# Performance work log

Measured on AMD Instinct MI355X. Metric: run time of the kernel, lower is better.

The kernel has to match this reference:

```python
import math
import jax, jax.numpy as jnp
import numpy as np

N = 50000   # nodes
E = 200000  # edges
B = 1024    # graphs
D = 256     # d_model
DA = 128    # d_atom_embed
DB = 64     # d_bond_embed
NA = 16     # num_atom_types
NB = 5      # num_bond_types
L = 6       # num_layers
DC = 2      # d_cond
IN0 = DA + 8 + D  # 392, layer-0 input dim


def setup_inputs() -> dict:
    key = jax.random.key(0)
    ks = jax.random.split(key, 48)
    def w(i, shape):
        fan_in = shape[-2] if len(shape) >= 2 else shape[-1]
        return jax.random.normal(ks[i], shape, jnp.float32) / jnp.sqrt(jnp.float32(fan_in))
    inp = {
        'x_noisy': jax.random.randint(ks[0], (N,), 0, NA),
        'node_mask_obs': jax.random.randint(ks[1], (N,), 0, 2),
        'edge_attr_noisy': jax.random.randint(ks[2], (E,), 0, NB),
        'edge_mask_obs': jax.random.randint(ks[3], (E,), 0, 2),
        'edge_index': jax.random.randint(ks[4], (2, E), 0, N),
        't_node': jax.random.randint(ks[5], (N,), 0, 200),
        'cond_vec': jax.random.normal(ks[6], (B, DC), jnp.float32),
        'batch': jnp.sort(jax.random.randint(ks[7], (N,), 0, B)),
        # embeddings
        'atom_emb': w(8, (NA, DA)), 'bond_emb': w(9, (NB, DB)),
        'nmask_emb': w(10, (2, 8)), 'emask_emb': w(11, (2, 8)),
        # timestep MLP
        't_W1': w(12, (D, D)), 't_b1': jnp.zeros((D,)),
        't_W2': w(13, (D, D)), 't_b2': jnp.zeros((D,)),
        # cond projection
        'cond_W': w(14, (DC, D)), 'cond_b': jnp.zeros((D,)),
        # edge MLP
        'edge_W1': w(15, (DB + 8, D)), 'edge_b1': jnp.zeros((D,)),
        'edge_W2': w(16, (D, D)), 'edge_b2': jnp.zeros((D,)),
        # layer-0 edge projection (GINEConv edge_dim -> in_dim)
        'e0_W': w(17, (D, IN0)),
        # layer-0 GINEConv MLP
        'conv0_W1': w(18, (IN0, D)), 'conv0_b1': jnp.zeros((D,)),
        'conv0_W2': w(19, (D, D)), 'conv0_b2': jnp.zeros((D,)),
        'conv0_eps': jnp.zeros(()),
        # layers 1..5 GINEConv MLPs (stacked)
        'convs_W1': w(20, (L - 1, D, D)), 'convs_b1': jnp.zeros((L - 1, D)),
        'convs_W2': w(21, (L - 1, D, D)), 'convs_b2': jnp.zeros((L - 1, D)),
        'convs_eps': jnp.zeros((L - 1,)),
        # BatchNorm (eval mode: running_mean=0, running_var=1)
        'bn_gamma': jnp.ones((L, D)) + 0.1 * jax.random.normal(ks[22], (L, D), jnp.float32),
        'bn_beta': 0.1 * jax.random.normal(ks[23], (L, D), jnp.float32),
        # heads
        'atom_W': w(24, (D, NA)), 'atom_b': jnp.zeros((NA,)),
        'bond_W': w(25, (D, NB)), 'bond_b': jnp.zeros((NB,)),
    }
    return inp


def _sinusoidal(t, d_model):
    half = d_model // 2
    freqs = jnp.exp(jnp.arange(half, dtype=jnp.float32) * (-math.log(10000.0) / max(1, half - 1)))
    angles = t.astype(jnp.float32)[:, None] * freqs[None, :]
    return jnp.concatenate([jnp.sin(angles), jnp.cos(angles)], axis=1)


def _bn_eval(h, gamma, beta, eps=1e-5):
    # running_mean=0, running_var=1
    return h * (gamma / jnp.sqrt(1.0 + eps)) + beta


def reference(x_noisy, node_mask_obs, edge_attr_noisy, edge_mask_obs, edge_index,
              t_node, cond_vec, batch,
              atom_emb, bond_emb, nmask_emb, emask_emb,
              t_W1, t_b1, t_W2, t_b2, cond_W, cond_b,
              edge_W1, edge_b1, edge_W2, edge_b2, e0_W,
              conv0_W1, conv0_b1, conv0_W2, conv0_b2, conv0_eps,
              convs_W1, convs_b1, convs_W2, convs_b2, convs_eps,
              bn_gamma, bn_beta, atom_W, atom_b, bond_W, bond_b):
    silu = jax.nn.silu
    # node features
    x_atom = atom_emb[x_noisy]                       # [N, DA]
    x_mask = nmask_emb[node_mask_obs]                # [N, 8]
    t_emb = _sinusoidal(t_node, D)                   # [N, D]
    t_emb = silu(t_emb @ t_W1 + t_b1) @ t_W2 + t_b2
    c_node = (cond_vec @ cond_W + cond_b)[batch]     # [N, D]
    h = jnp.concatenate([x_atom, x_mask, t_emb + c_node], axis=-1)  # [N, IN0]
    # edge features
    e_in = jnp.concatenate([bond_emb[edge_attr_noisy], emask_emb[edge_mask_obs]], axis=-1)
    e_feat = silu(e_in @ edge_W1 + edge_b1) @ edge_W2 + edge_b2      # [E, D]
    src, dst = edge_index[0], edge_index[1]

    def gine(h, e, eps, W1, b1, W2, b2):
        msg = jax.nn.relu(h[src] + e)                               # [E, d]
        agg = jax.ops.segment_sum(msg, dst, num_segments=N)          # [N, d]
        z = (1.0 + eps) * h + agg
        return silu(z @ W1 + b1) @ W2 + b2

    # layer 0 (edge features projected to IN0)
    h = gine(h, e_feat @ e0_W, conv0_eps, conv0_W1, conv0_b1, conv0_W2, conv0_b2)
    h = silu(_bn_eval(h, bn_gamma[0], bn_beta[0]))  # dropout off (eval)
    # layers 1..5
    for i in range(L - 1):
        h = gine(h, e_feat, convs_eps[i], convs_W1[i], convs_b1[i], convs_W2[i], convs_b2[i])
        h = silu(_bn_eval(h, bn_gamma[i + 1], bn_beta[i + 1]))
    atom_logits = h @ atom_W + atom_b                # [N, NA]
    edge_h = h[src] + h[dst]                          # [E, D]
    bond_logits = edge_h @ bond_W + bond_b            # [E, NB]
    return atom_logits, bond_logits
```

## Files before the change

kernel.cpp:

```cpp
#include <hip/hip_runtime.h>
#include <cstdint>
#include <cmath>

typedef unsigned short u16;
typedef unsigned int   u32;

using bf16x8 = __attribute__((ext_vector_type(8))) short;
using f32x4  = __attribute__((ext_vector_type(4))) float;

#define DM 256
#define W0 448
#define W0_REAL 392

__device__ __forceinline__ float bf2f(u16 v) {
  union { u32 u; float f; } c; c.u = ((u32)v) << 16; return c.f;
}
__device__ __forceinline__ u16 f2bf(float f) {
  union { float f; u32 u; } c; c.f = f;
  u32 u = c.u;
  return (u16)((u + 0x7FFFu + ((u >> 16) & 1u)) >> 16);
}
__device__ __forceinline__ float siluf(float y) {
  return y / (1.0f + __expf(-y));
}
__device__ __forceinline__ uint4 pack8(float f0, float f1, float f2, float f3,
                                       float f4, float f5, float f6, float f7) {
  uint4 o;
  o.x = (u32)f2bf(f0) | ((u32)f2bf(f1) << 16);
  o.y = (u32)f2bf(f2) | ((u32)f2bf(f3) << 16);
  o.z = (u32)f2bf(f4) | ((u32)f2bf(f5) << 16);
  o.w = (u32)f2bf(f6) | ((u32)f2bf(f7) << 16);
  return o;
}
__device__ __forceinline__ void acc8(float4& lo, float4& hi, uint4 hv,
                                     float4 ea, float4 eb) {
  lo.x += fmaxf(bf2f((u16)(hv.x & 0xFFFF)) + ea.x, 0.f);
  lo.y += fmaxf(bf2f((u16)(hv.x >> 16))    + ea.y, 0.f);
  lo.z += fmaxf(bf2f((u16)(hv.y & 0xFFFF)) + ea.z, 0.f);
  lo.w += fmaxf(bf2f((u16)(hv.y >> 16))    + ea.w, 0.f);
  hi.x += fmaxf(bf2f((u16)(hv.z & 0xFFFF)) + eb.x, 0.f);
  hi.y += fmaxf(bf2f((u16)(hv.z >> 16))    + eb.y, 0.f);
  hi.z += fmaxf(bf2f((u16)(hv.w & 0xFFFF)) + eb.z, 0.f);
  hi.w += fmaxf(bf2f((u16)(hv.w >> 16))    + eb.w, 0.f);
}

__global__ void wT_kernel(const float* __restrict__ W, u16* __restrict__ out,
                          int nmat, int K, int Kpad, int Nc) {
  int idx = blockIdx.x * 256 + threadIdx.x;
  int tot = nmat * Nc * Kpad;
  if (idx >= tot) return;
  int m = idx / (Nc * Kpad);
  int r = idx - m * (Nc * Kpad);
  int n = r / Kpad;
  int k = r - n * Kpad;
  float v = (k < K) ? W[(size_t)m * K * Nc + (size_t)k * Nc + n] : 0.0f;
  out[idx] = f2bf(v);
}

__global__ void whead_kernel(const float* __restrict__ atomW, const float* __restrict__ bondW,
                             u16* __restrict__ out) {
  int idx = blockIdx.x * 256 + threadIdx.x;
  if (idx >= 32 * 256) return;
  int j = idx >> 8, k = idx & 255;
  float v = 0.0f;
  if (j < 16) v = atomW[k * 16 + j];
  else if (j < 21) v = bondW[k * 5 + (j - 16)];
  out[idx] = f2bf(v);
}

__global__ void t_table_kernel(const float* __restrict__ W1, const float* __restrict__ b1,
                               const float* __restrict__ W2, const float* __restrict__ b2,
                               float* __restrict__ out) {
  __shared__ float s[256];
  __shared__ float a1[256];
  int r = blockIdx.x, t = threadIdx.x;
  float tv = (float)r;
// ... 117 lines not shown
  tmp[tid] = v;
  __syncthreads();
  for (int o = 1; o < 256; o <<= 1) {
    int t = (tid >= o) ? tmp[tid - o] : 0;
    __syncthreads();
    tmp[tid] += t;
    __syncthreads();
  }
  if (tid < nb) bsum[tid] = tmp[tid] - v;
}

__global__ void scan3_kernel(int* __restrict__ ro, int* __restrict__ cur,
                             const int* __restrict__ bsum, int N, int E) {
  int i = blockIdx.x * 256 + threadIdx.x;
  if (i < N) {
    int r = ro[i] + bsum[blockIdx.x];
    ro[i] = r;
    cur[i] = r;
  }
  if (i == 0) ro[N] = E;
}

__global__ void fill_kernel(const int* __restrict__ src, const int* __restrict__ dst,
                            const int* __restrict__ ea, const int* __restrict__ em,
                            int* __restrict__ cur, int* __restrict__ csr, int E) {
  int e = blockIdx.x * 256 + threadIdx.x;
  if (e < E) {
    int d = dst[e];
    int pos = atomicAdd(&cur[d], 1);
    csr[pos] = src[e] | ((ea[e] * 2 + em[e]) << 20);
  }
}

__global__ __launch_bounds__(256) void agg_z256(
    const u16* __restrict__ h, const float* __restrict__ etab,
    const int* __restrict__ ro, const int* __restrict__ csr,
    const float* __restrict__ epsp, u16* __restrict__ z, int N) {
  int wid = threadIdx.x >> 6, lane = threadIdx.x & 63;
  int n = blockIdx.x * 4 + wid;
  if (n >= N) return;
  int s0 = ro[n], s1 = ro[n + 1];
  float eps1 = 1.0f + *epsp;
  int half = lane >> 5, li = lane & 31;
  int c8 = li * 8;
  float4 aLo = {0, 0, 0, 0}, aHi = {0, 0, 0, 0};

  for (int base = s0; base < s1; base += 64) {
    int m = s1 - base; if (m > 64) m = 64;
    int pk = (lane < m) ? csr[base + lane] : 0;
    int j = 0;
    for (; j + 3 < m; j += 4) {
      int p0 = __shfl(pk, j + half);
      int p1 = __shfl(pk, j + 2 + half);
      uint4 h0v = *(const uint4*)(h + (size_t)(p0 & 0xFFFFF) * 256 + c8);
      uint4 h1v = *(const uint4*)(h + (size_t)(p1 & 0xFFFFF) * 256 + c8);
      const float* e0p = etab + (size_t)(p0 >> 20) * 256 + c8;
      const float* e1p = etab + (size_t)(p1 >> 20) * 256 + c8;
      float4 e0a = *(const float4*)e0p, e0b = *(const float4*)(e0p + 4);
      float4 e1a = *(const float4*)e1p, e1b = *(const float4*)(e1p + 4);
      acc8(aLo, aHi, h0v, e0a, e0b);
      acc8(aLo, aHi, h1v, e1a, e1b);
    }
    for (; j < m; j += 2) {
      int idx = j + half;
      bool act = idx < m;
      int p = __shfl(pk, act ? idx : (m - 1));
      uint4 hv = *(const uint4*)(h + (size_t)(p & 0xFFFFF) * 256 + c8);
      const float* ep = etab + (size_t)(p >> 20) * 256 + c8;
      float4 ea = *(const float4*)ep, eb = *(const float4*)(ep + 4);
      if (act) acc8(aLo, aHi, hv, ea, eb);
    }
  }
  aLo.x += __shfl(aLo.x, li + 32); aLo.y += __shfl(aLo.y, li + 32);
  aLo.z += __shfl(aLo.z, li + 32); aLo.w += __shfl(aLo.w, li + 32);
  aHi.x += __shfl(aHi.x, li + 32); aHi.y += __shfl(aHi.y, li + 32);
  aHi.z += __shfl(aHi.z, li + 32); aHi.w += __shfl(aHi.w, li + 32);
  if (half == 0) {
    uint4 hn = *(const uint4*)(h + (size_t)n * 256 + c8);
    uint4 o = pack8(
        eps1 * bf2f((u16)(hn.x & 0xFFFF)) + aLo.x,
        eps1 * bf2f((u16)(hn.x >> 16))    + aLo.y,
        eps1 * bf2f((u16)(hn.y & 0xFFFF)) + aLo.z,
        eps1 * bf2f((u16)(hn.y >> 16))    + aLo.w,
        eps1 * bf2f((u16)(hn.z & 0xFFFF)) + aHi.x,
        eps1 * bf2f((u16)(hn.z >> 16))    + aHi.y,
        eps1 * bf2f((u16)(hn.w & 0xFFFF)) + aHi.z,
        eps1 * bf2f((u16)(hn.w >> 16))    + aHi.w);
    *(uint4*)(z + (size_t)n * 256 + c8) = o;
  }
}

__global__ __launch_bounds__(256) void agg_z448(
    const u16* __restrict__ h, const float* __restrict__ etab,
    const int* __restrict__ ro, const int* __restrict__ csr,
    const float* __restrict__ epsp, u16* __restrict__ z, int N) {
  int wid = threadIdx.x >> 6, lane = threadIdx.x & 63;
  int n = blockIdx.x * 4 + wid;
  if (n >= N) return;
  int s0 = ro[n], s1 = ro[n + 1];
  float eps1 = 1.0f + *epsp;
  bool live = lane < 56;
  int c8 = live ? lane * 8 : 440;
  float4 aLo = {0, 0, 0, 0}, aHi = {0, 0, 0, 0};

  for (int base = s0; base < s1; base += 64) {
    int m = s1 - base; if (m > 64) m = 64;
    int pk = (lane < m) ? csr[base + lane] : 0;
    int j = 0;
    for (; j + 1 < m; j += 2) {
      int p0 = __shfl(pk, j);
      int p1 = __shfl(pk, j + 1);
      uint4 h0v = *(const uint4*)(h + (size_t)(p0 & 0xFFFFF) * W0 + c8);
      uint4 h1v = *(const uint4*)(h + (size_t)(p1 & 0xFFFFF) * W0 + c8);
      const float* e0p = etab + (size_t)(p0 >> 20) * W0 + c8;
      const float* e1p = etab + (size_t)(p1 >> 20) * W0 + c8;
      float4 e0a = *(const float4*)e0p, e0b = *(const float4*)(e0p + 4);
      float4 e1a = *(const float4*)e1p, e1b = *(const float4*)(e1p + 4);
      acc8(aLo, aHi, h0v, e0a, e0b);
      acc8(aLo, aHi, h1v, e1a, e1b);
    }
    if (j < m) {
      int p = __shfl(pk, j);
      uint4 hv = *(const uint4*)(h + (size_t)(p & 0xFFFFF) * W0 + c8);
      const float* ep = etab + (size_t)(p >> 20) * W0 + c8;
      float4 ea = *(const float4*)ep, eb = *(const float4*)(ep + 4);
      acc8(aLo, aHi, hv, ea, eb);
    }
  }
  if (live) {
    uint4 hn = *(const uint4*)(h + (size_t)n * W0 + c8);
    uint4 o = pack8(
        eps1 * bf2f((u16)(hn.x & 0xFFFF)) + aLo.x,
        eps1 * bf2f((u16)(hn.x >> 16))    + aLo.y,
        eps1 * bf2f((u16)(hn.y & 0xFFFF)) + aLo.z,
        eps1 * bf2f((u16)(hn.y >> 16))    + aLo.w,
        eps1 * bf2f((u16)(hn.z & 0xFFFF)) + aHi.x,
        eps1 * bf2f((u16)(hn.z >> 16))    + aHi.y,
        eps1 * bf2f((u16)(hn.w & 0xFFFF)) + aHi.z,
        eps1 * bf2f((u16)(hn.w >> 16))    + aHi.w);
    *(uint4*)(z + (size_t)n * W0 + c8) = o;
  }
}

__device__ __forceinline__ void g2l16(const u16* g, u16* l) {
  __builtin_amdgcn_global_load_lds(
      (__attribute__((address_space(1))) u32*)g,
      (__attribute__((address_space(3))) u32*)l, 16, 0, 0);
}

__global__ __launch_bounds__(256, 2) void gemm_fused(
    const u16* __restrict__ A, const u16* __restrict__ BT,
    const float* __restrict__ bias, const float* __restrict__ scale,
    const float* __restrict__ shift, u16* __restrict__ C, int M, int K) {
  __shared__ __align__(16) u16 smem[32768];
  u16* lA = smem;
  u16* lB = smem + 8192;
  int tid = threadIdx.x;
  int wid = tid >> 6, lane = tid & 63;
  int q = lane >> 4, rr = lane & 15;
  int wm = wid >> 1, wn = wid & 1;
  int m0 = blockIdx.x * 128;
  int lr = lane >> 3;
  int swz = (lane & 7) ^ (lr & 7);

  f32x4 acc[4][8] = {};

  for (int k0 = 0; k0 < K; k0 += 64) {
#pragma unroll
    for (int p = 0; p < 4; ++p) {
      int idx = wid * 4 + p;
      int gr = m0 + idx * 8 + lr;
      if (gr >= M) gr = M - 1;
      g2l16(A + (size_t)gr * K + k0 + swz * 8, lA + idx * 512);
    }
#pragma unroll
    for (int p = 0; p < 8; ++p) {
      int idx = wid * 8 + p;
      int nr = idx * 8 + lr;
      g2l16(BT + (size_t)nr * K + k0 + swz * 8, lB + idx * 512);
    }
    __syncthreads();
#pragma unroll
    for (int ks = 0; ks < 2; ++ks) {
      int ch = (ks << 2) | q;
      int slot = (ch ^ (rr & 7)) << 3;
      bf16x8 af[4], bf[8];
#pragma unroll
      for (int mt = 0; mt < 4; ++mt)
        af[mt] = *(const bf16x8*)&lA[(wm * 64 + mt * 16 + rr) * 64 + slot];
#pragma unroll
      for (int nt = 0; nt < 8; ++nt)
        bf[nt] = *(const bf16x8*)&lB[(wn * 128 + nt * 16 + rr) * 64 + slot];
#pragma unroll
      for (int mt = 0; mt < 4; ++mt)
#pragma unroll
        for (int nt = 0; nt < 8; ++nt)
          acc[mt][nt] = __builtin_amdgcn_mfma_f32_16x16x32_bf16(af[mt], bf[nt], acc[mt][nt], 0, 0, 0);
    }
    __syncthreads();
  }

  u16* slice = smem + wid * 8192;
#pragma unroll
  for (int nt = 0; nt < 8; ++nt) {
    int c = wn * 128 + nt * 16 + rr;
    float b = bias[c];
    float sc = scale ? scale[c] * 0.9999950000374997f : 1.0f;
    float sh = shift ? shift[c] : 0.0f;
#pragma unroll
    for (int mt = 0; mt < 4; ++mt)
#pragma unroll
      for (int i = 0; i < 4; ++i) {
        float y = (acc[mt][nt][i] + b) * sc + sh;
        slice[(mt * 16 + q * 4 + i) * 128 + nt * 16 + rr] = f2bf(siluf(y));
      }
  }
  __syncthreads();
  int rbase = m0 + wm * 64;
  int cbase = wn * 128;
#pragma unroll
  for (int j = 0; j < 16; ++j) {
    int idx = j * 64 + lane;
    int rloc = idx >> 4;
    int c8 = (idx & 15) * 8;
    if (rbase + rloc < M)
      *(uint4*)(C + (size_t)(rbase + rloc) * 256 + cbase + c8) =
          *(const uint4*)(slice + rloc * 128 + c8);
  }
}

__global__ __launch_bounds__(256) void head_gemm(
    const u16* __restrict__ A, const u16* __restrict__ WT,
    const float* __restrict__ atomB,
    float* __restrict__ atom_out, float* __restrict__ P, int M) {
  __shared__ __align__(16) u16 lA[128 * 32];
  __shared__ __align__(16) u16 lB[32 * 264];
  int tid = threadIdx.x;
  int wid = tid >> 6, lane = tid & 63;
  int q = lane >> 4, rr = lane & 15;
  int m0 = blockIdx.x * 128;

  for (int i = tid; i < 32 * 256; i += 256)
    lB[(i >> 8) * 264 + (i & 255)] = WT[i];

  f32x4 acc[2][2] = {};
  int arow = tid >> 2, acol = (tid & 3) * 8;

  for (int k0 = 0; k0 < 256; k0 += 32) {
#pragma unroll
    for (int p = 0; p < 2; ++p) {
      int gr = m0 + p * 64 + arow;
      if (gr >= M) gr = M - 1;
      g2l16(A + (size_t)gr * 256 + k0 + acol, &lA[p * 2048 + wid * 512]);
    }
    __syncthreads();
    bf16x8 af[2], bfr[2];
#pragma unroll
    for (int mt = 0; mt < 2; ++mt)
      af[mt] = *(const bf16x8*)&lA[(wid * 32 + mt * 16 + rr) * 32 + q * 8];
#pragma unroll
// ... 85 lines not shown
  const float* edge_b2   = (const float*)d_in[21];
  const float* e0_W      = (const float*)d_in[22];
  const float* conv0_W1  = (const float*)d_in[23];
  const float* conv0_b1  = (const float*)d_in[24];
  const float* conv0_W2  = (const float*)d_in[25];
  const float* conv0_b2  = (const float*)d_in[26];
  const float* conv0_eps = (const float*)d_in[27];
  const float* convs_W1  = (const float*)d_in[28];
  const float* convs_b1  = (const float*)d_in[29];
  const float* convs_W2  = (const float*)d_in[30];
  const float* convs_b2  = (const float*)d_in[31];
  const float* convs_eps = (const float*)d_in[32];
  const float* bn_gamma  = (const float*)d_in[33];
  const float* bn_beta   = (const float*)d_in[34];
  const float* atom_W    = (const float*)d_in[35];
  const float* atom_b    = (const float*)d_in[36];
  const float* bond_W    = (const float*)d_in[37];
  const float* bond_b    = (const float*)d_in[38];

  const int N = in_sizes[0];
  const int E = in_sizes[2];
  const int B = in_sizes[6] / 2;
  const int* srcp = eidx;
  const int* dstp = eidx + E;

  char* base = (char*)d_ws;
  size_t off = 0;
  auto alloc = [&](size_t bytes) -> char* {
    char* p = base + off;
    off = (off + bytes + 255) & ~(size_t)255;
    return p;
  };
  u16* h0   = (u16*)alloc((size_t)N * W0 * 2);
  u16* z0   = (u16*)alloc((size_t)N * W0 * 2);
  u16* ubuf = (u16*)alloc((size_t)N * DM * 2);
  u16* w10t = (u16*)alloc((size_t)DM * W0 * 2);
  u16* w20t = (u16*)alloc((size_t)DM * DM * 2);
  u16* wc1t = (u16*)alloc((size_t)5 * DM * DM * 2);
  u16* wc2t = (u16*)alloc((size_t)5 * DM * DM * 2);
  u16* wht  = (u16*)alloc((size_t)32 * DM * 2);
  float* ttab  = (float*)alloc((size_t)200 * DM * 4);
  float* cprojb= (float*)alloc((size_t)B * DM * 4);
  float* eftab = (float*)alloc((size_t)10 * DM * 4);
  float* e0tab = (float*)alloc((size_t)10 * W0 * 4);
  float* Pbuf  = (float*)alloc((size_t)N * 8 * 4);
  int* deg  = (int*)alloc((size_t)N * 4);
  int* ro   = (int*)alloc((size_t)(N + 1) * 4);
  int* cur  = (int*)alloc((size_t)N * 4);
  int* csr  = (int*)alloc((size_t)E * 4);
  int* bsum = (int*)alloc((size_t)256 * 4);
  (void)ws_size; (void)n_in; (void)out_size;

  u16* hbuf = h0;
  u16* zbuf = z0;
  float* atom_out = (float*)d_out;
  float* bond_out = atom_out + (size_t)N * 16;

  hipMemsetAsync(deg, 0, (size_t)N * 4, stream);

  wT_kernel<<<(DM * W0 + 255) / 256, 256, 0, stream>>>(conv0_W1, w10t, 1, W0_REAL, W0, DM);
  wT_kernel<<<(DM * DM + 255) / 256, 256, 0, stream>>>(conv0_W2, w20t, 1, DM, DM, DM);
  wT_kernel<<<(5 * DM * DM + 255) / 256, 256, 0, stream>>>(convs_W1, wc1t, 5, DM, DM, DM);
  wT_kernel<<<(5 * DM * DM + 255) / 256, 256, 0, stream>>>(convs_W2, wc2t, 5, DM, DM, DM);
  whead_kernel<<<32, 256, 0, stream>>>(atom_W, bond_W, wht);
  t_table_kernel<<<200, 256, 0, stream>>>(t_W1, t_b1, t_W2, t_b2, ttab);
  cproj_kernel<<<(B * DM + 255) / 256, 256, 0, stream>>>(cvec, cond_W, cond_b, cprojb, B);
  ef_tab_kernel<<<10, 256, 0, stream>>>(bond_emb, emask_emb, edge_W1, edge_b1, edge_W2, edge_b2, eftab);
  e0_tab_kernel<<<10, 512, 0, stream>>>(eftab, e0_W, e0tab);
  h0_kernel<<<(N * 56 + 255) / 256, 256, 0, stream>>>(x_noisy, nmaskobs, tnode, batch,
      atom_emb, nmask_emb, ttab, cprojb, h0, N);
  const int nscan = (N + 255) / 256;
  deg_kernel<<<(E + 255) / 256, 256, 0, stream>>>(dstp, deg, E);
  scan1_kernel<<<nscan, 256, 0, stream>>>(deg, ro, bsum, N);
  scan2_kernel<<<1, 256, 0, stream>>>(bsum, nscan);
  scan3_kernel<<<nscan, 256, 0, stream>>>(ro, cur, bsum, N, E);
  fill_kernel<<<(E + 255) / 256, 256, 0, stream>>>(srcp, dstp, ea, em, cur, csr, E);

  const int ggrid = (N + 127) / 128;
  const int nagg = (N + 3) / 4;
  agg_z448<<<nagg, 256, 0, stream>>>(h0, e0tab, ro, csr, conv0_eps, z0, N);
  gemm_fused<<<ggrid, 256, 0, stream>>>(z0, w10t, conv0_b1, nullptr, nullptr, ubuf, N, W0);
  gemm_fused<<<ggrid, 256, 0, stream>>>(ubuf, w20t, conv0_b2, bn_gamma, bn_beta, hbuf, N, DM);
  for (int i = 0; i < 5; ++i) {
    agg_z256<<<nagg, 256, 0, stream>>>(hbuf, eftab, ro, csr, convs_eps + i, zbuf, N);
    gemm_fused<<<ggrid, 256, 0, stream>>>(zbuf, wc1t + (size_t)i * DM * DM, convs_b1 + i * DM,
                                          nullptr, nullptr, ubuf, N, DM);
    gemm_fused<<<ggrid, 256, 0, stream>>>(ubuf, wc2t + (size_t)i * DM * DM, convs_b2 + i * DM,
                                          bn_gamma + (i + 1) * DM, bn_beta + (i + 1) * DM, hbuf, N, DM);
  }
  head_gemm<<<(N + 127) / 128, 256, 0, stream>>>(hbuf, wht, atom_b, atom_out, Pbuf, N);
  bond_edge<<<(E + 255) / 256, 256, 0, stream>>>(Pbuf, srcp, dstp, bond_b, bond_out, E);
}
```

Measured before the change: 676.4 us.

## Fuse GINE aggregation and both MLP GEMMs into one per-layer kernel

Each GINE layer's neighbor aggregation, first GEMM with SiLU, and second GEMM with BatchNorm and SiLU now run in one kernel. The aggregated z tile and the intermediate activation stay in swizzled shared memory instead of going through global z and u buffers. This removes two global round-trips and two launches per layer. In exchange, tiles are smaller (64 or 32 rows), so weights are reloaded more often per row, and the gather phase and MFMA phase run serially within a block, which may limit latency hiding.

```diff
diff --git a/kernel.cpp b/kernel.cpp
--- a/kernel.cpp
+++ b/kernel.cpp
@@ -42,6 +42,14 @@
   hi.y += fmaxf(bf2f((u16)(hv.z >> 16))    + eb.y, 0.f);
   hi.z += fmaxf(bf2f((u16)(hv.w & 0xFFFF)) + eb.z, 0.f);
   hi.w += fmaxf(bf2f((u16)(hv.w >> 16))    + eb.w, 0.f);
+}
+__device__ __forceinline__ void g2l16(const u16* g, u16* l) {
+  __builtin_amdgcn_global_load_lds(
+      (__attribute__((address_space(1))) u32*)g,
+      (__attribute__((address_space(3))) u32*)l, 16, 0, 0);
+}
+__device__ __forceinline__ int swzpos(int j, int r) {
+  return ((j & ~7) | ((j & 7) ^ (r & 7))) << 3;
 }
 
 __global__ void wT_kernel(const float* __restrict__ W, u16* __restrict__ out,
@@ -225,200 +233,335 @@
   }
 }
 
-__global__ __launch_bounds__(256) void agg_z256(
-    const u16* __restrict__ h, const float* __restrict__ etab,
+__global__ __launch_bounds__(256, 2) void layerN_fused(
+    const u16* __restrict__ hin, const float* __restrict__ etab,
     const int* __restrict__ ro, const int* __restrict__ csr,
-    const float* __restrict__ epsp, u16* __restrict__ z, int N) {
-  int wid = threadIdx.x >> 6, lane = threadIdx.x & 63;
-  int n = blockIdx.x * 4 + wid;
-  if (n >= N) return;
-  int s0 = ro[n], s1 = ro[n + 1];
-  float eps1 = 1.0f + *epsp;
-  int half = lane >> 5, li = lane & 31;
-  int c8 = li * 8;
-  float4 aLo = {0, 0, 0, 0}, aHi = {0, 0, 0, 0};
-
-  for (int base = s0; base < s1; base += 64) {
-    int m = s1 - base; if (m > 64) m = 64;
-    int pk = (lane < m) ? csr[base + lane] : 0;
-    int j = 0;
-    for (; j + 3 < m; j += 4) {
-      int p0 = __shfl(pk, j + half);
-      int p1 = __shfl(pk, j + 2 + half);
-      uint4 h0v = *(const uint4*)(h + (size_t)(p0 & 0xFFFFF) * 256 + c8);
-      uint4 h1v = *(const uint4*)(h + (size_t)(p1 & 0xFFFFF) * 256 + c8);
-      const float* e0p = etab + (size_t)(p0 >> 20) * 256 + c8;
-      const float* e1p = etab + (size_t)(p1 >> 20) * 256 + c8;
-      float4 e0a = *(const float4*)e0p, e0b = *(const float4*)(e0p + 4);
-      float4 e1a = *(const float4*)e1p, e1b = *(const float4*)(e1p + 4);
-      acc8(aLo, aHi, h0v, e0a, e0b);
-      acc8(aLo, aHi, h1v, e1a, e1b);
-    }
-    for (; j < m; j += 2) {
-      int idx = j + half;
-      bool act = idx < m;
-      int p = __shfl(pk, act ? idx : (m - 1));
-      uint4 hv = *(const uint4*)(h + (size_t)(p & 0xFFFFF) * 256 + c8);
-      const float* ep = etab + (size_t)(p >> 20) * 256 + c8;
-      float4 ea = *(const float4*)ep, eb = *(const float4*)(ep + 4);
-      if (act) acc8(aLo, aHi, hv, ea, eb);
-    }
-  }
-  aLo.x += __shfl(aLo.x, li + 32); aLo.y += __shfl(aLo.y, li + 32);
-  aLo.z += __shfl(aLo.z, li + 32); aLo.w += __shfl(aLo.w, li + 32);
-  aHi.x += __shfl(aHi.x, li + 32); aHi.y += __shfl(aHi.y, li + 32);
-  aHi.z += __shfl(aHi.z, li + 32); aHi.w += __shfl(aHi.w, li + 32);
-  if (half == 0) {
-    uint4 hn = *(const uint4*)(h + (size_t)n * 256 + c8);
-    uint4 o = pack8(
-        eps1 * bf2f((u16)(hn.x & 0xFFFF)) + aLo.x,
-        eps1 * bf2f((u16)(hn.x >> 16))    + aLo.y,
-        eps1 * bf2f((u16)(hn.y & 0xFFFF)) + aLo.z,
-        eps1 * bf2f((u16)(hn.y >> 16))    + aLo.w,
-        eps1 * bf2f((u16)(hn.z & 0xFFFF)) + aHi.x,
-        eps1 * bf2f((u16)(hn.z >> 16))    + aHi.y,
-        eps1 * bf2f((u16)(hn.w & 0xFFFF)) + aHi.z,
-        eps1 * bf2f((u16)(hn.w >> 16))    + aHi.w);
-    *(uint4*)(z + (size_t)n * 256 + c8) = o;
-  }
-}
-
-__global__ __launch_bounds__(256) void agg_z448(
-    const u16* __restrict__ h, const float* __restrict__ etab,
-    const int* __restrict__ ro, const int* __restrict__ csr,
-    const float* __restrict__ epsp, u16* __restrict__ z, int N) {
-  int wid = threadIdx.x >> 6, lane = threadIdx.x & 63;
-  int n = blockIdx.x * 4 + wid;
-  if (n >= N) return;
-  int s0 = ro[n], s1 = ro[n + 1];
-  float eps1 = 1.0f + *epsp;
-  bool live = lane < 56;
-  int c8 = live ? lane * 8 : 440;
-  float4 aLo = {0, 0, 0, 0}, aHi = {0, 0, 0, 0};
-
-  for (int base = s0; base < s1; base += 64) {
-    int m = s1 - base; if (m > 64) m = 64;
-    int pk = (lane < m) ? csr[base + lane] : 0;
-    int j = 0;
-    for (; j + 1 < m; j += 2) {
-      int p0 = __shfl(pk, j);
-      int p1 = __shfl(pk, j + 1);
-      uint4 h0v = *(const uint4*)(h + (size_t)(p0 & 0xFFFFF) * W0 + c8);
-      uint4 h1v = *(const uint4*)(h + (size_t)(p1 & 0xFFFFF) * W0 + c8);
-      const float* e0p = etab + (size_t)(p0 >> 20) * W0 + c8;
-      const float* e1p = etab + (size_t)(p1 >> 20) * W0 + c8;
-      float4 e0a = *(const float4*)e0p, e0b = *(const float4*)(e0p + 4);
-      float4 e1a = *(const float4*)e1p, e1b = *(const float4*)(e1p + 4);
-      acc8(aLo, aHi, h0v, e0a, e0b);
-      acc8(aLo, aHi, h1v, e1a, e1b);
-    }
-    if (j < m) {
-      int p = __shfl(pk, j);
-      uint4 hv = *(const uint4*)(h + (size_t)(p & 0xFFFFF) * W0 + c8);
-      const float* ep = etab + (size_t)(p >> 20) * W0 + c8;
-      float4 ea = *(const float4*)ep, eb = *(const float4*)(ep + 4);
-      acc8(aLo, aHi, hv, ea, eb);
-    }
-  }
-  if (live) {
-    uint4 hn = *(const uint4*)(h + (size_t)n * W0 + c8);
-    uint4 o = pack8(
-        eps1 * bf2f((u16)(hn.x & 0xFFFF)) + aLo.x,
-        eps1 * bf2f((u16)(hn.x >> 16))    + aLo.y,
-        eps1 * bf2f((u16)(hn.y & 0xFFFF)) + aLo.z,
-        eps1 * bf2f((u16)(hn.y >> 16))    + aLo.w,
-        eps1 * bf2f((u16)(hn.z & 0xFFFF)) + aHi.x,
-        eps1 * bf2f((u16)(hn.z >> 16))    + aHi.y,
-        eps1 * bf2f((u16)(hn.w & 0xFFFF)) + aHi.z,
-        eps1 * bf2f((u16)(hn.w >> 16))    + aHi.w);
-    *(uint4*)(z + (size_t)n * W0 + c8) = o;
-  }
-}
-
-__device__ __forceinline__ void g2l16(const u16* g, u16* l) {
-  __builtin_amdgcn_global_load_lds(
-      (__attribute__((address_space(1))) u32*)g,
-      (__attribute__((address_space(3))) u32*)l, 16, 0, 0);
-}
-
-__global__ __launch_bounds__(256, 2) void gemm_fused(
-    const u16* __restrict__ A, const u16* __restrict__ BT,
-    const float* __restrict__ bias, const float* __restrict__ scale,
-    const float* __restrict__ shift, u16* __restrict__ C, int M, int K) {
+    const float* __restrict__ epsp,
+    const u16* __restrict__ W1T, const float* __restrict__ b1,
+    const u16* __restrict__ W2T, const float* __restrict__ b2,
+    const float* __restrict__ gamma, const float* __restrict__ beta,
+    u16* __restrict__ hout, int N) {
   __shared__ __align__(16) u16 smem[32768];
-  u16* lA = smem;
-  u16* lB = smem + 8192;
+  u16* zA = smem;
+  u16* lB = smem + 16384;
   int tid = threadIdx.x;
   int wid = tid >> 6, lane = tid & 63;
+  int m0 = blockIdx.x * 64;
+  float eps1 = 1.0f + *epsp;
+
+  {
+    int half = lane >> 5, li = lane & 31;
+    int c8 = li * 8;
+    for (int i = 0; i < 16; ++i) {
+      int r = wid * 16 + i;
+      int n = m0 + r;
+      if (n >= N) break;
+      int s0 = ro[n], s1 = ro[n + 1];
+      float4 aLo = {0, 0, 0, 0}, aHi = {0, 0, 0, 0};
+      for (int base = s0; base < s1; base += 64) {
+        int m = s1 - base; if (m > 64) m = 64;
+        int pk = (lane < m) ? csr[base + lane] : 0;
+        int j = 0;
+        for (; j + 3 < m; j += 4) {
+          int p0 = __shfl(pk, j + half);
+          int p1 = __shfl(pk, j + 2 + half);
+          uint4 h0v = *(const uint4*)(hin + (size_t)(p0 & 0xFFFFF) * 256 + c8);
+          uint4 h1v = *(const uint4*)(hin + (size_t)(p1 & 0xFFFFF) * 256 + c8);
+          const float* e0p = etab + (size_t)(p0 >> 20) * 256 + c8;
+          const float* e1p = etab + (size_t)(p1 >> 20) * 256 + c8;
+          float4 e0a = *(const float4*)e0p, e0b = *(const float4*)(e0p + 4);
+          float4 e1a = *(const float4*)e1p, e1b = *(const float4*)(e1p + 4);
+          acc8(aLo, aHi, h0v, e0a, e0b);
+          acc8(aLo, aHi, h1v, e1a, e1b);
+        }
+        for (; j < m; j += 2) {
+          int idx = j + half;
+          bool act = idx < m;
+          int p = __shfl(pk, act ? idx : (m - 1));
+          uint4 hv = *(const uint4*)(hin + (size_t)(p & 0xFFFFF) * 256 + c8);
+          const float* ep = etab + (size_t)(p >> 20) * 256 + c8;
+          float4 ea = *(const float4*)ep, eb = *(const float4*)(ep + 4);
+          if (act) acc8(aLo, aHi, hv, ea, eb);
+        }
+      }
+      aLo.x += __shfl(aLo.x, li + 32); aLo.y += __shfl(aLo.y, li + 32);
+      aLo.z += __shfl(aLo.z, li + 32); aLo.w += __shfl(aLo.w, li + 32);
+      aHi.x += __shfl(aHi.x, li + 32); aHi.y += __shfl(aHi.y, li + 32);
+      aHi.z += __shfl(aHi.z, li + 32); aHi.w += __shfl(aHi.w, li + 32);
+      if (half == 0) {
+        uint4 hn = *(const uint4*)(hin + (size_t)n * 256 + c8);
+        uint4 o = pack8(
+            eps1 * bf2f((u16)(hn.x & 0xFFFF)) + aLo.x,
+            eps1 * bf2f((u16)(hn.x >> 16))    + aLo.y,
+            eps1 * bf2f((u16)(hn.y & 0xFFFF)) + aLo.z,
+            eps1 * bf2f((u16)(hn.y >> 16))    + aLo.w,
+            eps1 * bf2f((u16)(hn.z & 0xFFFF)) + aHi.x,
+            eps1 * bf2f((u16)(hn.z >> 16))    + aHi.y,
+            eps1 * bf2f((u16)(hn.w & 0xFFFF)) + aHi.z,
+            eps1 * bf2f((u16)(hn.w >> 16))    + aHi.w);
+        *(uint4*)(zA + r * 256 + swzpos(li, r)) = o;
+      }
+    }
+  }
+  __syncthreads();
+
   int q = lane >> 4, rr = lane & 15;
   int wm = wid >> 1, wn = wid & 1;
-  int m0 = blockIdx.x * 128;
-  int lr = lane >> 3;
-  int swz = (lane & 7) ^ (lr & 7);
-
-  f32x4 acc[4][8] = {};
-
-  for (int k0 = 0; k0 < K; k0 += 64) {
-#pragma unroll
-    for (int p = 0; p < 4; ++p) {
-      int idx = wid * 4 + p;
-      int gr = m0 + idx * 8 + lr;
-      if (gr >= M) gr = M - 1;
-      g2l16(A + (size_t)gr * K + k0 + swz * 8, lA + idx * 512);
-    }
+  int lr8 = lane >> 3;
+  int swz = (lane & 7) ^ (lr8 & 7);
+  f32x4 acc[2][8];
+
+#pragma unroll
+  for (int mt = 0; mt < 2; ++mt)
+#pragma unroll
+    for (int nt = 0; nt < 8; ++nt) acc[mt][nt] = (f32x4){0, 0, 0, 0};
+  for (int k0 = 0; k0 < 256; k0 += 64) {
 #pragma unroll
     for (int p = 0; p < 8; ++p) {
       int idx = wid * 8 + p;
-      int nr = idx * 8 + lr;
-      g2l16(BT + (size_t)nr * K + k0 + swz * 8, lB + idx * 512);
+      int nr = idx * 8 + lr8;
+      g2l16(W1T + (size_t)nr * 256 + k0 + swz * 8, lB + idx * 512);
     }
     __syncthreads();
 #pragma unroll
     for (int ks = 0; ks < 2; ++ks) {
-      int ch = (ks << 2) | q;
-      int slot = (ch ^ (rr & 7)) << 3;
-      bf16x8 af[4], bf[8];
-#pragma unroll
-      for (int mt = 0; mt < 4; ++mt)
-        af[mt] = *(const bf16x8*)&lA[(wm * 64 + mt * 16 + rr) * 64 + slot];
+      int slot = ((ks * 4 + q) ^ (rr & 7)) << 3;
+      bf16x8 af[2], bfv[8];
+#pragma unroll
+      for (int mt = 0; mt < 2; ++mt)
+        af[mt] = *(const bf16x8*)&zA[(wm * 32 + mt * 16 + rr) * 256 + k0 + slot];
 #pragma unroll
       for (int nt = 0; nt < 8; ++nt)
-        bf[nt] = *(const bf16x8*)&lB[(wn * 128 + nt * 16 + rr) * 64 + slot];
-#pragma unroll
-      for (int mt = 0; mt < 4; ++mt)
+        bfv[nt] = *(const bf16x8*)&lB[(wn * 128 + nt * 16 + rr) * 64 + slot];
+#pragma unroll
+      for (int mt = 0; mt < 2; ++mt)
 #pragma unroll
         for (int nt = 0; nt < 8; ++nt)
-          acc[mt][nt] = __builtin_amdgcn_mfma_f32_16x16x32_bf16(af[mt], bf[nt], acc[mt][nt], 0, 0, 0);
-    }
-    __syncthreads();
-  }
-
-  u16* slice = smem + wid * 8192;
+          acc[mt][nt] = __builtin_amdgcn_mfma_f32_16x16x32_bf16(af[mt], bfv[nt], acc[mt][nt], 0, 0, 0);
+    }
+    __syncthreads();
+  }
 #pragma unroll
   for (int nt = 0; nt < 8; ++nt) {
     int c = wn * 128 + nt * 16 + rr;
-    float b = bias[c];
-    float sc = scale ? scale[c] * 0.9999950000374997f : 1.0f;
-    float sh = shift ? shift[c] : 0.0f;
-#pragma unroll
-    for (int mt = 0; mt < 4; ++mt)
+    float bb = b1[c];
+    int j = c >> 3;
+#pragma unroll
+    for (int mt = 0; mt < 2; ++mt)
 #pragma unroll
       for (int i = 0; i < 4; ++i) {
-        float y = (acc[mt][nt][i] + b) * sc + sh;
-        slice[(mt * 16 + q * 4 + i) * 128 + nt * 16 + rr] = f2bf(siluf(y));
-      }
-  }
-  __syncthreads();
-  int rbase = m0 + wm * 64;
-  int cbase = wn * 128;
-#pragma unroll
-  for (int j = 0; j < 16; ++j) {
-    int idx = j * 64 + lane;
-    int rloc = idx >> 4;
-    int c8 = (idx & 15) * 8;
-    if (rbase + rloc < M)
-      *(uint4*)(C + (size_t)(rbase + rloc) * 256 + cbase + c8) =
-          *(const uint4*)(slice + rloc * 128 + c8);
+        int r = wm * 32 + mt * 16 + q * 4 + i;
+        zA[r * 256 + swzpos(j, r) + (c & 7)] = f2bf(siluf(acc[mt][nt][i] + bb));
+      }
+  }
+  __syncthreads();
+
+#pragma unroll
+  for (int mt = 0; mt < 2; ++mt)
+#pragma unroll
+    for (int nt = 0; nt < 8; ++nt) acc[mt][nt] = (f32x4){0, 0, 0, 0};
+  for (int k0 = 0; k0 < 256; k0 += 64) {
+#pragma unroll
+    for (int p = 0; p < 8; ++p) {
+      int idx = wid * 8 + p;
+      int nr = idx * 8 + lr8;
+      g2l16(W2T + (size_t)nr * 256 + k0 + swz * 8, lB + idx * 512);
+    }
+    __syncthreads();
+#pragma unroll
+    for (int ks = 0; ks < 2; ++ks) {
+      int slot = ((ks * 4 + q) ^ (rr & 7)) << 3;
+      bf16x8 af[2], bfv[8];
+#pragma unroll
+      for (int mt = 0; mt < 2; ++mt)
+        af[mt] = *(const bf16x8*)&zA[(wm * 32 + mt * 16 + rr) * 256 + k0 + slot];
+#pragma unroll
+      for (int nt = 0; nt < 8; ++nt)
+        bfv[nt] = *(const bf16x8*)&lB[(wn * 128 + nt * 16 + rr) * 64 + slot];
+#pragma unroll
+      for (int mt = 0; mt < 2; ++mt)
+#pragma unroll
+        for (int nt = 0; nt < 8; ++nt)
+          acc[mt][nt] = __builtin_amdgcn_mfma_f32_16x16x32_bf16(af[mt], bfv[nt], acc[mt][nt], 0, 0, 0);
+    }
+    __syncthreads();
+  }
+#pragma unroll
+  for (int nt = 0; nt < 8; ++nt) {
+    int c = wn * 128 + nt * 16 + rr;
+    float bb = b2[c];
+    float sc = gamma[c] * 0.9999950000374997f;
+    float sh = beta[c];
+#pragma unroll
+    for (int mt = 0; mt < 2; ++mt)
+#pragma unroll
+      for (int i = 0; i < 4; ++i) {
+        int r = wm * 32 + mt * 16 + q * 4 + i;
+        float y = (acc[mt][nt][i] + bb) * sc + sh;
+        lB[r * 256 + c] = f2bf(siluf(y));
+      }
+  }
+  __syncthreads();
+#pragma unroll
+  for (int it = 0; it < 8; ++it) {
+    int idx = it * 256 + tid;
+    int r = idx >> 5, c16 = idx & 31;
+    if (m0 + r < N)
+      *(uint4*)(hout + (size_t)(m0 + r) * 256 + c16 * 8) =
+          *(const uint4*)(lB + r * 256 + c16 * 8);
+  }
+}
+
+__global__ __launch_bounds__(256, 2) void layer0_fused(
+    const u16* __restrict__ hin, const float* __restrict__ etab,
+    const int* __restrict__ ro, const int* __restrict__ csr,
+    const float* __restrict__ epsp,
+    const u16* __restrict__ W1T, const float* __restrict__ b1,
+    const u16* __restrict__ W2T, const float* __restrict__ b2,
+    const float* __restrict__ gamma, const float* __restrict__ beta,
+    u16* __restrict__ hout, int N) {
+  __shared__ __align__(16) u16 smem[30720];
+  u16* zA = smem;
+  u16* lB = smem + 14336;
+  int tid = threadIdx.x;
+  int wid = tid >> 6, lane = tid & 63;
+  int m0 = blockIdx.x * 32;
+  float eps1 = 1.0f + *epsp;
+
+  {
+    bool live = lane < 56;
+    int c8 = live ? lane * 8 : 440;
+    for (int i = 0; i < 8; ++i) {
+      int r = wid * 8 + i;
+      int n = m0 + r;
+      if (n >= N) break;
+      int s0 = ro[n], s1 = ro[n + 1];
+      float4 aLo = {0, 0, 0, 0}, aHi = {0, 0, 0, 0};
+      for (int base = s0; base < s1; base += 64) {
+        int m = s1 - base; if (m > 64) m = 64;
+        int pk = (lane < m) ? csr[base + lane] : 0;
+        int j = 0;
+        for (; j + 1 < m; j += 2) {
+          int p0 = __shfl(pk, j);
+          int p1 = __shfl(pk, j + 1);
+          uint4 h0v = *(const uint4*)(hin + (size_t)(p0 & 0xFFFFF) * W0 + c8);
+          uint4 h1v = *(const uint4*)(hin + (size_t)(p1 & 0xFFFFF) * W0 + c8);
+          const float* e0p = etab + (size_t)(p0 >> 20) * W0 + c8;
+          const float* e1p = etab + (size_t)(p1 >> 20) * W0 + c8;
+          float4 e0a = *(const float4*)e0p, e0b = *(const float4*)(e0p + 4);
+          float4 e1a = *(const float4*)e1p, e1b = *(const float4*)(e1p + 4);
+          acc8(aLo, aHi, h0v, e0a, e0b);
+          acc8(aLo, aHi, h1v, e1a, e1b);
+        }
+        if (j < m) {
+          int p = __shfl(pk, j);
+          uint4 hv = *(const uint4*)(hin + (size_t)(p & 0xFFFFF) * W0 + c8);
+          const float* ep = etab + (size_t)(p >> 20) * W0 + c8;
+          float4 ea = *(const float4*)ep, eb = *(const float4*)(ep + 4);
+          acc8(aLo, aHi, hv, ea, eb);
+        }
+      }
+      if (live) {
+        uint4 hn = *(const uint4*)(hin + (size_t)n * W0 + c8);
+        uint4 o = pack8(
+            eps1 * bf2f((u16)(hn.x & 0xFFFF)) + aLo.x,
+            eps1 * bf2f((u16)(hn.x >> 16))    + aLo.y,
+            eps1 * bf2f((u16)(hn.y & 0xFFFF)) + aLo.z,
+            eps1 * bf2f((u16)(hn.y >> 16))    + aLo.w,
+            eps1 * bf2f((u16)(hn.z & 0xFFFF)) + aHi.x,
+            eps1 * bf2f((u16)(hn.z >> 16))    + aHi.y,
+            eps1 * bf2f((u16)(hn.w & 0xFFFF)) + aHi.z,
+            eps1 * bf2f((u16)(hn.w >> 16))    + aHi.w);
+        *(uint4*)(zA + r * 448 + swzpos(lane, r)) = o;
+      }
+    }
+  }
+  __syncthreads();
+
+  int q = lane >> 4, rr = lane & 15;
+  int wm = wid >> 1, wn = wid & 1;
+  int lr8 = lane >> 3;
+  int swz = (lane & 7) ^ (lr8 & 7);
+  f32x4 acc[8];
+
+#pragma unroll
+  for (int nt = 0; nt < 8; ++nt) acc[nt] = (f32x4){0, 0, 0, 0};
+  for (int k0 = 0; k0 < 448; k0 += 64) {
+#pragma unroll
+    for (int p = 0; p < 8; ++p) {
+      int idx = wid * 8 + p;
+      int nr = idx * 8 + lr8;
+      g2l16(W1T + (size_t)nr * 448 + k0 + swz * 8, lB + idx * 512);
+    }
+    __syncthreads();
+#pragma unroll
+    for (int ks = 0; ks < 2; ++ks) {
+      int slot = ((ks * 4 + q) ^ (rr & 7)) << 3;
+      bf16x8 af = *(const bf16x8*)&zA[(wm * 16 + rr) * 448 + k0 + slot];
+#pragma unroll
+      for (int nt = 0; nt < 8; ++nt) {
+        bf16x8 bfv = *(const bf16x8*)&lB[(wn * 128 + nt * 16 + rr) * 64 + slot];
+        acc[nt] = __builtin_amdgcn_mfma_f32_16x16x32_bf16(af, bfv, acc[nt], 0, 0, 0);
+      }
+    }
+    __syncthreads();
+  }
+#pragma unroll
+  for (int nt = 0; nt < 8; ++nt) {
+    int c = wn * 128 + nt * 16 + rr;
+    float bb = b1[c];
+    int j = c >> 3;
+#pragma unroll
+    for (int i = 0; i < 4; ++i) {
+      int r = wm * 16 + q * 4 + i;
+      zA[r * 256 + swzpos(j, r) + (c & 7)] = f2bf(siluf(acc[nt][i] + bb));
+    }
+  }
+  __syncthreads();
+
+#pragma unroll
+  for (int nt = 0; nt < 8; ++nt) acc[nt] = (f32x4){0, 0, 0, 0};
+  for (int k0 = 0; k0 < 256; k0 += 64) {
+#pragma unroll
+    for (int p = 0; p < 8; ++p) {
+      int idx = wid * 8 + p;
+      int nr = idx * 8 + lr8;
+      g2l16(W2T + (size_t)nr * 256 + k0 + swz * 8, lB + idx * 512);
+    }
+    __syncthreads();
+#pragma unroll
+    for (int ks = 0; ks < 2; ++ks) {
+      int slot = ((ks * 4 + q) ^ (rr & 7)) << 3;
+      bf16x8 af = *(const bf16x8*)&zA[(wm * 16 + rr) * 256 + k0 + slot];
+#pragma unroll
+      for (int nt = 0; nt < 8; ++nt) {
+        bf16x8 bfv = *(const bf16x8*)&lB[(wn * 128 + nt * 16 + rr) * 64 + slot];
+        acc[nt] = __builtin_amdgcn_mfma_f32_16x16x32_bf16(af, bfv, acc[nt], 0, 0, 0);
+      }
+    }
+    __syncthreads();
+  }
+#pragma unroll
+  for (int nt = 0; nt < 8; ++nt) {
+    int c = wn * 128 + nt * 16 + rr;
+    float bb = b2[c];
+    float sc = gamma[c] * 0.9999950000374997f;
+    float sh = beta[c];
+#pragma unroll
+    for (int i = 0; i < 4; ++i) {
+      int r = wm * 16 + q * 4 + i;
+      float y = (acc[nt][i] + bb) * sc + sh;
+      lB[r * 256 + c] = f2bf(siluf(y));
+    }
+  }
+  __syncthreads();
+#pragma unroll
+  for (int it = 0; it < 4; ++it) {
+    int idx = it * 256 + tid;
+    int r = idx >> 5, c16 = idx & 31;
+    if (m0 + r < N)
+      *(uint4*)(hout + (size_t)(m0 + r) * 256 + c16 * 8) =
+          *(const uint4*)(lB + r * 256 + c16 * 8);
   }
 }
 
@@ -570,8 +713,8 @@
     return p;
   };
   u16* h0   = (u16*)alloc((size_t)N * W0 * 2);
-  u16* z0   = (u16*)alloc((size_t)N * W0 * 2);
-  u16* ubuf = (u16*)alloc((size_t)N * DM * 2);
+  u16* hA   = (u16*)alloc((size_t)N * DM * 2);
+  u16* hB   = (u16*)alloc((size_t)N * DM * 2);
   u16* w10t = (u16*)alloc((size_t)DM * W0 * 2);
   u16* w20t = (u16*)alloc((size_t)DM * DM * 2);
   u16* wc1t = (u16*)alloc((size_t)5 * DM * DM * 2);
@@ -589,8 +732,6 @@
   int* bsum = (int*)alloc((size_t)256 * 4);
   (void)ws_size; (void)n_in; (void)out_size;
 
-  u16* hbuf = h0;
-  u16* zbuf = z0;
   float* atom_out = (float*)d_out;
   float* bond_out = atom_out + (size_t)N * 16;
 
@@ -614,18 +755,17 @@
   scan3_kernel<<<nscan, 256, 0, stream>>>(ro, cur, bsum, N, E);
   fill_kernel<<<(E + 255) / 256, 256, 0, stream>>>(srcp, dstp, ea, em, cur, csr, E);
 
-  const int ggrid = (N + 127) / 128;
-  const int nagg = (N + 3) / 4;
-  agg_z448<<<nagg, 256, 0, stream>>>(h0, e0tab, ro, csr, conv0_eps, z0, N);
-  gemm_fused<<<ggrid, 256, 0, stream>>>(z0, w10t, conv0_b1, nullptr, nullptr, ubuf, N, W0);
-  gemm_fused<<<ggrid, 256, 0, stream>>>(ubuf, w20t, conv0_b2, bn_gamma, bn_beta, hbuf, N, DM);
+  layer0_fused<<<(N + 31) / 32, 256, 0, stream>>>(h0, e0tab, ro, csr, conv0_eps,
+      w10t, conv0_b1, w20t, conv0_b2, bn_gamma, bn_beta, hA, N);
+  u16* hc = hA;
+  u16* hn = hB;
   for (int i = 0; i < 5; ++i) {
-    agg_z256<<<nagg, 256, 0, stream>>>(hbuf, eftab, ro, csr, convs_eps + i, zbuf, N);
-    gemm_fused<<<ggrid, 256, 0, stream>>>(zbuf, wc1t + (size_t)i * DM * DM, convs_b1 + i * DM,
-                                          nullptr, nullptr, ubuf, N, DM);
-    gemm_fused<<<ggrid, 256, 0, stream>>>(ubuf, wc2t + (size_t)i * DM * DM, convs_b2 + i * DM,
-                                          bn_gamma + (i + 1) * DM, bn_beta + (i + 1) * DM, hbuf, N, DM);
-  }
-  head_gemm<<<(N + 127) / 128, 256, 0, stream>>>(hbuf, wht, atom_b, atom_out, Pbuf, N);
+    layerN_fused<<<(N + 63) / 64, 256, 0, stream>>>(hc, eftab, ro, csr, convs_eps + i,
+        wc1t + (size_t)i * DM * DM, convs_b1 + i * DM,
+        wc2t + (size_t)i * DM * DM, convs_b2 + i * DM,
+        bn_gamma + (i + 1) * DM, bn_beta + (i + 1) * DM, hn, N);
+    u16* t = hc; hc = hn; hn = t;
+  }
+  head_gemm<<<(N + 127) / 128, 256, 0, stream>>>(hc, wht, atom_b, atom_out, Pbuf, N);
   bond_edge<<<(E + 255) / 256, 256, 0, stream>>>(Pbuf, srcp, dstp, bond_b, bond_out, E);
 }
```

New measurement: 836.0 us. 1.24x slower.

## Shrink GEMM M-tile to 64 rows and deepen gather unroll in aggregation

Applied to the files above, without the earlier changes.

The fused GEMM now uses 64-row tiles instead of 128, halving accumulator registers and shrinking LDS so three blocks can share a CU, and it doubles the grid size. The epilogue staging is rewritten to write a full 64x256 tile into shared memory and store it row-wise. Both aggregation kernels unroll the neighbor gather loop twice as deep to keep more independent loads in flight. The trade-off is lower B-tile reuse per block (B is reloaded for every 64 rows) and higher register pressure in the gather loops.

```diff
diff --git a/kernel.cpp b/kernel.cpp
--- a/kernel.cpp
+++ b/kernel.cpp
@@ -42,6 +42,11 @@
   hi.y += fmaxf(bf2f((u16)(hv.z >> 16))    + eb.y, 0.f);
   hi.z += fmaxf(bf2f((u16)(hv.w & 0xFFFF)) + eb.z, 0.f);
   hi.w += fmaxf(bf2f((u16)(hv.w >> 16))    + eb.w, 0.f);
+}
+__device__ __forceinline__ void g2l16(const u16* g, u16* l) {
+  __builtin_amdgcn_global_load_lds(
+      (__attribute__((address_space(1))) u32*)g,
+      (__attribute__((address_space(3))) u32*)l, 16, 0, 0);
 }
 
 __global__ void wT_kernel(const float* __restrict__ W, u16* __restrict__ out,
@@ -242,17 +247,27 @@
     int m = s1 - base; if (m > 64) m = 64;
     int pk = (lane < m) ? csr[base + lane] : 0;
     int j = 0;
-    for (; j + 3 < m; j += 4) {
+    for (; j + 7 < m; j += 8) {
       int p0 = __shfl(pk, j + half);
       int p1 = __shfl(pk, j + 2 + half);
+      int p2 = __shfl(pk, j + 4 + half);
+      int p3 = __shfl(pk, j + 6 + half);
       uint4 h0v = *(const uint4*)(h + (size_t)(p0 & 0xFFFFF) * 256 + c8);
       uint4 h1v = *(const uint4*)(h + (size_t)(p1 & 0xFFFFF) * 256 + c8);
+      uint4 h2v = *(const uint4*)(h + (size_t)(p2 & 0xFFFFF) * 256 + c8);
+      uint4 h3v = *(const uint4*)(h + (size_t)(p3 & 0xFFFFF) * 256 + c8);
       const float* e0p = etab + (size_t)(p0 >> 20) * 256 + c8;
       const float* e1p = etab + (size_t)(p1 >> 20) * 256 + c8;
+      const float* e2p = etab + (size_t)(p2 >> 20) * 256 + c8;
+      const float* e3p = etab + (size_t)(p3 >> 20) * 256 + c8;
       float4 e0a = *(const float4*)e0p, e0b = *(const float4*)(e0p + 4);
       float4 e1a = *(const float4*)e1p, e1b = *(const float4*)(e1p + 4);
+      float4 e2a = *(const float4*)e2p, e2b = *(const float4*)(e2p + 4);
+      float4 e3a = *(const float4*)e3p, e3b = *(const float4*)(e3p + 4);
       acc8(aLo, aHi, h0v, e0a, e0b);
       acc8(aLo, aHi, h1v, e1a, e1b);
+      acc8(aLo, aHi, h2v, e2a, e2b);
+      acc8(aLo, aHi, h3v, e3a, e3b);
     }
     for (; j < m; j += 2) {
       int idx = j + half;
@@ -300,19 +315,29 @@
     int m = s1 - base; if (m > 64) m = 64;
     int pk = (lane < m) ? csr[base + lane] : 0;
     int j = 0;
-    for (; j + 1 < m; j += 2) {
+    for (; j + 3 < m; j += 4) {
       int p0 = __shfl(pk, j);
       int p1 = __shfl(pk, j + 1);
+      int p2 = __shfl(pk, j + 2);
+      int p3 = __shfl(pk, j + 3);
       uint4 h0v = *(const uint4*)(h + (size_t)(p0 & 0xFFFFF) * W0 + c8);
       uint4 h1v = *(const uint4*)(h + (size_t)(p1 & 0xFFFFF) * W0 + c8);
+      uint4 h2v = *(const uint4*)(h + (size_t)(p2 & 0xFFFFF) * W0 + c8);
+      uint4 h3v = *(const uint4*)(h + (size_t)(p3 & 0xFFFFF) * W0 + c8);
       const float* e0p = etab + (size_t)(p0 >> 20) * W0 + c8;
       const float* e1p = etab + (size_t)(p1 >> 20) * W0 + c8;
+      const float* e2p = etab + (size_t)(p2 >> 20) * W0 + c8;
+      const float* e3p = etab + (size_t)(p3 >> 20) * W0 + c8;
       float4 e0a = *(const float4*)e0p, e0b = *(const float4*)(e0p + 4);
       float4 e1a = *(const float4*)e1p, e1b = *(const float4*)(e1p + 4);
+      float4 e2a = *(const float4*)e2p, e2b = *(const float4*)(e2p + 4);
+      float4 e3a = *(const float4*)e3p, e3b = *(const float4*)(e3p + 4);
       acc8(aLo, aHi, h0v, e0a, e0b);
       acc8(aLo, aHi, h1v, e1a, e1b);
-    }
-    if (j < m) {
+      acc8(aLo, aHi, h2v, e2a, e2b);
+      acc8(aLo, aHi, h3v, e3a, e3b);
+    }
+    for (; j < m; ++j) {
       int p = __shfl(pk, j);
       uint4 hv = *(const uint4*)(h + (size_t)(p & 0xFFFFF) * W0 + c8);
       const float* ep = etab + (size_t)(p >> 20) * W0 + c8;
@@ -335,65 +360,58 @@
   }
 }
 
-__device__ __forceinline__ void g2l16(const u16* g, u16* l) {
-  __builtin_amdgcn_global_load_lds(
-      (__attribute__((address_space(1))) u32*)g,
-      (__attribute__((address_space(3))) u32*)l, 16, 0, 0);
-}
-
-__global__ __launch_bounds__(256, 2) void gemm_fused(
+__global__ __launch_bounds__(256, 3) void gemm_fused(
     const u16* __restrict__ A, const u16* __restrict__ BT,
     const float* __restrict__ bias, const float* __restrict__ scale,
     const float* __restrict__ shift, u16* __restrict__ C, int M, int K) {
-  __shared__ __align__(16) u16 smem[32768];
+  __shared__ __align__(16) u16 smem[20480];
   u16* lA = smem;
-  u16* lB = smem + 8192;
+  u16* lB = smem + 4096;
   int tid = threadIdx.x;
   int wid = tid >> 6, lane = tid & 63;
   int q = lane >> 4, rr = lane & 15;
   int wm = wid >> 1, wn = wid & 1;
-  int m0 = blockIdx.x * 128;
-  int lr = lane >> 3;
-  int swz = (lane & 7) ^ (lr & 7);
-
-  f32x4 acc[4][8] = {};
+  int m0 = blockIdx.x * 64;
+  int lr8 = lane >> 3;
+  int swz = (lane & 7) ^ (lr8 & 7);
+
+  f32x4 acc[2][8] = {};
 
   for (int k0 = 0; k0 < K; k0 += 64) {
 #pragma unroll
-    for (int p = 0; p < 4; ++p) {
-      int idx = wid * 4 + p;
-      int gr = m0 + idx * 8 + lr;
+    for (int p = 0; p < 2; ++p) {
+      int idx = wid * 2 + p;
+      int gr = m0 + idx * 8 + lr8;
       if (gr >= M) gr = M - 1;
       g2l16(A + (size_t)gr * K + k0 + swz * 8, lA + idx * 512);
     }
 #pragma unroll
     for (int p = 0; p < 8; ++p) {
       int idx = wid * 8 + p;
-      int nr = idx * 8 + lr;
+      int nr = idx * 8 + lr8;
       g2l16(BT + (size_t)nr * K + k0 + swz * 8, lB + idx * 512);
     }
     __syncthreads();
 #pragma unroll
     for (int ks = 0; ks < 2; ++ks) {
-      int ch = (ks << 2) | q;
-      int slot = (ch ^ (rr & 7)) << 3;
-      bf16x8 af[4], bf[8];
-#pragma unroll
-      for (int mt = 0; mt < 4; ++mt)
-        af[mt] = *(const bf16x8*)&lA[(wm * 64 + mt * 16 + rr) * 64 + slot];
+      int slot = ((ks * 4 + q) ^ (rr & 7)) << 3;
+      bf16x8 af[2], bfv[8];
+#pragma unroll
+      for (int mt = 0; mt < 2; ++mt)
+        af[mt] = *(const bf16x8*)&lA[(wm * 32 + mt * 16 + rr) * 64 + slot];
 #pragma unroll
       for (int nt = 0; nt < 8; ++nt)
-        bf[nt] = *(const bf16x8*)&lB[(wn * 128 + nt * 16 + rr) * 64 + slot];
-#pragma unroll
-      for (int mt = 0; mt < 4; ++mt)
+        bfv[nt] = *(const bf16x8*)&lB[(wn * 128 + nt * 16 + rr) * 64 + slot];
+#pragma unroll
+      for (int mt = 0; mt < 2; ++mt)
 #pragma unroll
         for (int nt = 0; nt < 8; ++nt)
-          acc[mt][nt] = __builtin_amdgcn_mfma_f32_16x16x32_bf16(af[mt], bf[nt], acc[mt][nt], 0, 0, 0);
-    }
-    __syncthreads();
-  }
-
-  u16* slice = smem + wid * 8192;
+          acc[mt][nt] = __builtin_amdgcn_mfma_f32_16x16x32_bf16(af[mt], bfv[nt], acc[mt][nt], 0, 0, 0);
+    }
+    __syncthreads();
+  }
+
+  u16* lC = smem;
 #pragma unroll
   for (int nt = 0; nt < 8; ++nt) {
     int c = wn * 128 + nt * 16 + rr;
@@ -401,24 +419,22 @@
     float sc = scale ? scale[c] * 0.9999950000374997f : 1.0f;
     float sh = shift ? shift[c] : 0.0f;
 #pragma unroll
-    for (int mt = 0; mt < 4; ++mt)
+    for (int mt = 0; mt < 2; ++mt)
 #pragma unroll
       for (int i = 0; i < 4; ++i) {
+        int r = wm * 32 + mt * 16 + q * 4 + i;
         float y = (acc[mt][nt][i] + b) * sc + sh;
-        slice[(mt * 16 + q * 4 + i) * 128 + nt * 16 + rr] = f2bf(siluf(y));
+        lC[r * 256 + c] = f2bf(siluf(y));
       }
   }
   __syncthreads();
-  int rbase = m0 + wm * 64;
-  int cbase = wn * 128;
-#pragma unroll
-  for (int j = 0; j < 16; ++j) {
-    int idx = j * 64 + lane;
-    int rloc = idx >> 4;
-    int c8 = (idx & 15) * 8;
-    if (rbase + rloc < M)
-      *(uint4*)(C + (size_t)(rbase + rloc) * 256 + cbase + c8) =
-          *(const uint4*)(slice + rloc * 128 + c8);
+#pragma unroll
+  for (int it = 0; it < 8; ++it) {
+    int idx = it * 256 + tid;
+    int r = idx >> 5, c16 = idx & 31;
+    if (m0 + r < M)
+      *(uint4*)(C + (size_t)(m0 + r) * 256 + c16 * 8) =
+          *(const uint4*)(lC + r * 256 + c16 * 8);
   }
 }
 
@@ -614,7 +630,7 @@
   scan3_kernel<<<nscan, 256, 0, stream>>>(ro, cur, bsum, N, E);
   fill_kernel<<<(E + 255) / 256, 256, 0, stream>>>(srcp, dstp, ea, em, cur, csr, E);
 
-  const int ggrid = (N + 127) / 128;
+  const int ggrid = (N + 63) / 64;
   const int nagg = (N + 3) / 4;
   agg_z448<<<nagg, 256, 0, stream>>>(h0, e0tab, ro, csr, conv0_eps, z0, N);
   gemm_fused<<<ggrid, 256, 0, stream>>>(z0, w10t, conv0_b1, nullptr, nullptr, ubuf, N, W0);
```

Measured after the change: 771.2 us. 14.0% more time.
